# Optimization experiments

Hardware: AMD Instinct MI355X
Metric: run time of the kernel (lower is better)

Reference implementation:

```python
import jax, jax.numpy as jnp
from jax import lax
import numpy as np

B, T, IN_DIM = 32, 2048, 36
HIDDEN, CODE_DIM, N_CODES, STRIDE, N_RES = 256, 128, 1024, 4, 4
BETA = 0.25
GN_GROUPS = 8


def conv1d(x, w, b, stride=1, padding=0):
    # x: (B,C,T), w: (O,I,k) torch layout
    y = lax.conv_general_dilated(x, w, (stride,), [(padding, padding)],
                                 dimension_numbers=('NCH', 'OIH', 'NCH'))
    return y + b[None, :, None]


def conv_transpose1d(x, w, b, stride, padding):
    # torch ConvTranspose1d weight layout (in, out, k); output_padding=0 (stride even)
    k = w.shape[-1]
    w_t = jnp.transpose(jnp.flip(w, -1), (1, 0, 2))  # (out, in, k)
    y = lax.conv_general_dilated(x, w_t, (1,), [(k - 1 - padding, k - 1 - padding)],
                                 lhs_dilation=(stride,), dimension_numbers=('NCH', 'OIH', 'NCH'))
    return y + b[None, :, None]


def group_norm(x, gamma, beta, eps=1e-5):
    Bx, C, Tx = x.shape
    xg = x.reshape(Bx, GN_GROUPS, C // GN_GROUPS, Tx)
    mu = xg.mean(axis=(2, 3), keepdims=True)
    var = xg.var(axis=(2, 3), keepdims=True)
    xn = ((xg - mu) * lax.rsqrt(var + eps)).reshape(Bx, C, Tx)
    return xn * gamma[None, :, None] + beta[None, :, None]


def res_block(x, g1, be1, w1, b1, g2, be2, w2, b2):
    h = conv1d(jax.nn.silu(group_norm(x, g1, be1)), w1, b1, padding=1)
    h = conv1d(jax.nn.silu(group_norm(h, g2, be2)), w2, b2, padding=1)
    return x + h


def vq(z_e, codebook):
    # z_e: (B, C, K); nearest-neighbor + straight-through estimator
    Bx, C, K = z_e.shape
    z = z_e.transpose(0, 2, 1).reshape(-1, C)  # (B*K, C)
    dist = (z * z).sum(1, keepdims=True) + (codebook * codebook).sum(1)[None, :] - 2.0 * (z @ codebook.T)
    codes = jnp.argmin(dist, axis=1)  # (B*K,)
    z_q = codebook[codes].reshape(Bx, K, C).transpose(0, 2, 1)  # (B, C, K)
    z_q_st = z_e + lax.stop_gradient(z_q - z_e)
    loss_vq = jnp.mean((z_q - lax.stop_gradient(z_e)) ** 2) + BETA * jnp.mean((lax.stop_gradient(z_q) - z_e) ** 2)
    counts = jnp.zeros((N_CODES,), z_e.dtype).at[codes].add(1.0)
    avg = counts / z.shape[0]
    perplexity = jnp.exp(-jnp.sum(avg * jnp.log(avg + 1e-10)))
    return z_q_st, codes.reshape(Bx, K), loss_vq, perplexity


def _gather_pos(a):  # slices (0:18),(18:21),(27:30) -> 24 dims
    return jnp.concatenate([a[..., 0:18], a[..., 18:21], a[..., 27:30]], axis=-1)


def _gather_dir(a):  # slices (21:27),(30:36) -> 12 dims
    return jnp.concatenate([a[..., 21:27], a[..., 30:36]], axis=-1)


def setup_inputs() -> dict:
    ks = iter(jax.random.split(jax.random.key(0), 64))

    def nrm(shape, scale=1.0):
        return scale * jax.random.normal(next(ks), shape, jnp.float32)

    def cw(o, i, k):
        return nrm((o, i, k), 1.0 / np.sqrt(i * k))

    def rcw(n, o, i, k):
        return nrm((n, o, i, k), 1.0 / np.sqrt(i * k))

    inp = {
        'x': nrm((B, T, IN_DIM)),
        'hand_valid_mask': jax.random.uniform(next(ks), (B, T, 2), jnp.float32),
        'enc_in_w': cw(HIDDEN, IN_DIM, 3), 'enc_in_b': nrm((HIDDEN,), 0.01),
        'enc_gn1_g': 1.0 + nrm((N_RES, HIDDEN), 0.01), 'enc_gn1_b': nrm((N_RES, HIDDEN), 0.01),
        'enc_c1_w': rcw(N_RES, HIDDEN, HIDDEN, 3), 'enc_c1_b': nrm((N_RES, HIDDEN), 0.01),
        'enc_gn2_g': 1.0 + nrm((N_RES, HIDDEN), 0.01), 'enc_gn2_b': nrm((N_RES, HIDDEN), 0.01),
        'enc_c2_w': rcw(N_RES, HIDDEN, HIDDEN, 3), 'enc_c2_b': nrm((N_RES, HIDDEN), 0.01),
        'down_w': cw(HIDDEN, HIDDEN, 2 * STRIDE), 'down_b': nrm((HIDDEN,), 0.01),
        'enc_out_w': cw(CODE_DIM, HIDDEN, 1), 'enc_out_b': nrm((CODE_DIM,), 0.01),
        'codebook': jax.random.uniform(next(ks), (N_CODES, CODE_DIM), jnp.float32, -1.0 / N_CODES, 1.0 / N_CODES),
        'dec_in_w': cw(HIDDEN, CODE_DIM, 1), 'dec_in_b': nrm((HIDDEN,), 0.01),
        'up_w': nrm((HIDDEN, HIDDEN, 2 * STRIDE), 1.0 / np.sqrt(HIDDEN * 2 * STRIDE)), 'up_b': nrm((HIDDEN,), 0.01),
        'dec_gn1_g': 1.0 + nrm((N_RES, HIDDEN), 0.01), 'dec_gn1_b': nrm((N_RES, HIDDEN), 0.01),
        'dec_c1_w': rcw(N_RES, HIDDEN, HIDDEN, 3), 'dec_c1_b': nrm((N_RES, HIDDEN), 0.01),
        'dec_gn2_g': 1.0 + nrm((N_RES, HIDDEN), 0.01), 'dec_gn2_b': nrm((N_RES, HIDDEN), 0.01),
        'dec_c2_w': rcw(N_RES, HIDDEN, HIDDEN, 3), 'dec_c2_b': nrm((N_RES, HIDDEN), 0.01),
        'dec_out_w': cw(IN_DIM, HIDDEN, 3), 'dec_out_b': nrm((IN_DIM,), 0.01),
    }
    return inp


def reference(x, hand_valid_mask, enc_in_w, enc_in_b, enc_gn1_g, enc_gn1_b, enc_c1_w, enc_c1_b,
              enc_gn2_g, enc_gn2_b, enc_c2_w, enc_c2_b, down_w, down_b, enc_out_w, enc_out_b,
              codebook, dec_in_w, dec_in_b, up_w, up_b, dec_gn1_g, dec_gn1_b, dec_c1_w, dec_c1_b,
              dec_gn2_g, dec_gn2_b, dec_c2_w, dec_c2_b, dec_out_w, dec_out_b):
    Bx, Tx, _ = x.shape
    # ---- encode ----
    h = conv1d(x.transpose(0, 2, 1), enc_in_w, enc_in_b, padding=1)
    for i in range(N_RES):
        h = res_block(h, enc_gn1_g[i], enc_gn1_b[i], enc_c1_w[i], enc_c1_b[i],
                      enc_gn2_g[i], enc_gn2_b[i], enc_c2_w[i], enc_c2_b[i])
    h = conv1d(h, down_w, down_b, stride=STRIDE, padding=STRIDE // 2)
    z_e = conv1d(h, enc_out_w, enc_out_b)  # (B, CODE_DIM, K); latent mask is all-ones (no input_length)
    # ---- quantize ----
    z_q, codes, loss_vq, perplexity = vq(z_e, codebook)
    # ---- decode ----
    h = conv1d(z_q, dec_in_w, dec_in_b)
    h = conv_transpose1d(h, up_w, up_b, STRIDE, STRIDE // 2)
    for i in range(N_RES):
        h = res_block(h, dec_gn1_g[i], dec_gn1_b[i], dec_c1_w[i], dec_c1_b[i],
                      dec_gn2_g[i], dec_gn2_b[i], dec_c2_w[i], dec_c2_b[i])
    x_hat = conv1d(h, dec_out_w, dec_out_b, padding=1)[..., :Tx].transpose(0, 2, 1)  # (B,T,36)
    # ---- smooth-L1 position loss (mask of ones (B,T,1): denom = B*T) ----
    d = _gather_pos(x_hat) - _gather_pos(x)
    ad = jnp.abs(d)
    l1 = jnp.where(ad < 1.0, 0.5 * d * d, ad - 0.5)
    loss_recon_pos = l1.sum() / (Bx * Tx)
    # ---- cosine direction loss with hand validity mask ----
    x_vec = _gather_dir(x).reshape(Bx, Tx, 4, 3)
    h_vec = _gather_dir(x_hat).reshape(Bx, Tx, 4, 3)
    mL = hand_valid_mask[..., 0]
    mR = hand_valid_mask[..., 1]
    m_vec = jnp.stack([mL, mL, mR, mR], axis=-1)  # (B,T,4)
    eps = 1e-8
    xn = x_vec / (jnp.linalg.norm(x_vec, axis=-1, keepdims=True) + eps)
    hn = h_vec / (jnp.linalg.norm(h_vec, axis=-1, keepdims=True) + eps)
    cos = (xn * hn).sum(-1)
    loss_recon_dir = ((1.0 - cos) * m_vec).sum() / jnp.maximum(m_vec.sum(), 1.0)
    return x_hat, codes, loss_vq, perplexity, loss_recon_pos, loss_recon_dir
```

## Files before the change

kernel.cpp:

```cpp
#include <hip/hip_runtime.h>
#include <cstddef>
#include <cstdint>


#define TID ((int)threadIdx.x)
#define NB 32

__device__ __forceinline__ float silu_f(float y) { return y / (1.f + expf(-y)); }

__global__ void perm_oik_iko(const float* __restrict__ src, float* __restrict__ dst,
                             int R, int O, int I, int K) {
  int n = R * O * I * K;
  for (int idx = blockIdx.x * blockDim.x + TID; idx < n; idx += gridDim.x * blockDim.x) {
    int o = idx % O;
    int k = (idx / O) % K;
    int i = (idx / (O * K)) % I;
    int r = idx / (O * K * I);
    dst[idx] = src[((r * O + o) * I + i) * K + k];
  }
}

__global__ void perm_decout(const float* __restrict__ src, float* __restrict__ dst) {
  int n = 256 * 36 * 4;
  for (int idx = blockIdx.x * blockDim.x + TID; idx < n; idx += gridDim.x * blockDim.x) {
    int k = idx & 3;
    int o = (idx >> 2) % 36;
    int i = idx / 144;
    dst[idx] = (k < 3) ? src[(o * 256 + i) * 3 + k] : 0.f;
  }
}

__global__ void zero_k(float* p, int n) {
  int i = blockIdx.x * blockDim.x + TID;
  if (i < n) p[i] = 0.f;
}

__global__ void csq_f32(const float* __restrict__ cb, float* __restrict__ csq) {
  int j = blockIdx.x * blockDim.x + TID;
  if (j < 1024) {
    float s = 0.f;
    for (int c = 0; c < 128; c++) { float v = cb[j * 128 + c]; s += v * v; }
    csq[j] = s;
  }
}

__global__ __launch_bounds__(256) void conv_in_k(const float* __restrict__ x, const float* __restrict__ wT,
                                                 const float* __restrict__ bias, float* __restrict__ out,
                                                 float* __restrict__ partOut) {
  int b = blockIdx.x >> 5;
  int t0 = (blockIdx.x & 31) << 6;
  int o0 = blockIdx.y << 6;
  int tx = TID & 15, oy = TID >> 4;
  __shared__ float ins[36][68];
  __shared__ float wsl[36 * 192];
  for (int idx = TID; idx < 36 * 66; idx += 256) {
    int i = idx % 36, c = idx / 36;
    int t = t0 - 1 + c;
    float v = 0.f;
    if (t >= 0 && t < 2048) v = x[((size_t)(b * 2048 + t)) * 36 + i];
    ins[i][c] = v;
  }
  for (int idx = TID; idx < 36 * 192; idx += 256) {
    int o = idx & 63;
    int kk = (idx >> 6) % 3;
    int i = idx / 192;
    wsl[idx] = wT[(i * 3 + kk) * 256 + o0 + o];
  }
  __syncthreads();
  float acc[4][4];
#pragma unroll
  for (int m = 0; m < 4; m++)
#pragma unroll
    for (int n = 0; n < 4; n++) acc[m][n] = 0.f;
  for (int i = 0; i < 36; i++) {
    float xv[6];
    float4 x4 = *(const float4*)&ins[i][tx << 2];
    xv[0] = x4.x; xv[1] = x4.y; xv[2] = x4.z; xv[3] = x4.w;
    xv[4] = ins[i][(tx << 2) + 4];
    xv[5] = ins[i][(tx << 2) + 5];
    const float* wrow = &wsl[i * 192];
    float wv[3][4];
    *(float4*)wv[0] = *(const float4*)&wrow[oy << 2];
    *(float4*)wv[1] = *(const float4*)&wrow[64 + (oy << 2)];
    *(float4*)wv[2] = *(const float4*)&wrow[128 + (oy << 2)];
#pragma unroll
    for (int m = 0; m < 4; m++)
#pragma unroll
      for (int n = 0; n < 4; n++)
        acc[m][n] = fmaf(wv[0][m], xv[n], fmaf(wv[1][m], xv[n + 1], fmaf(wv[2][m], xv[n + 2], acc[m][n])));
  }
  int obase = o0 + (oy << 2);
  float s1 = 0.f, s2 = 0.f;
#pragma unroll
  for (int m = 0; m < 4; m++) {
    int o = obase + m;
    float bv = bias[o];
    size_t rowo = (((size_t)((b << 8) + o)) << 11) + t0 + (tx << 2);
#pragma unroll
    for (int n = 0; n < 4; n++) {
      float v = acc[m][n] + bv;
      out[rowo + n] = v;
      s1 += v; s2 += v * v;
    }
  }
  __syncthreads();
  float* red = (float*)ins;
  red[TID] = s1; red[256 + TID] = s2;
  __syncthreads();
  for (int st = 64; st > 0; st >>= 1) {
    if ((TID & 127) < st) { red[TID] += red[TID + st]; red[256 + TID] += red[256 + TID + st]; }
    __syncthreads();
  }
  if ((TID & 127) == 0) {
    int g = (blockIdx.y << 1) + (TID >> 7);
    atomicAdd(&partOut[(((b << 3) + g) << 1)], red[TID]);
    atomicAdd(&partOut[(((b << 3) + g) << 1) + 1], red[256 + TID]);
  }
}

__global__ __launch_bounds__(256, 2) void conv3_gn_k(const float* __restrict__ in, const float* __restrict__ partIn,
                                                     const float* __restrict__ gamma, const float* __restrict__ beta,
                                                     const float* __restrict__ wT, const float* __restrict__ bias,
                                                     const float* __restrict__ src, float* __restrict__ out,
                                                     float* __restrict__ partOut) {
  int b = blockIdx.x >> 3;
  int t0 = (blockIdx.x & 7) << 8;
  int o0 = blockIdx.y << 7;
  int tx = TID & 15, oy = TID >> 4;
  __shared__ float ins[16][264];
  __shared__ float wsl[3 * 16 * 128];
  float acc[2][4][16];
#pragma unroll
  for (int h = 0; h < 2; h++)
#pragma unroll
    for (int m = 0; m < 4; m++)
#pragma unroll
      for (int n = 0; n < 16; n++) acc[h][m][n] = 0.f;
  for (int ic0 = 0; ic0 < 256; ic0 += 16) {
    int g = ic0 >> 5;
    const float* pp = partIn + (((size_t)((b << 3) + g)) << 1);
    float s1 = pp[0], s2 = pp[1];
    float mu = s1 * (1.f / 65536.f);
    float var = s2 * (1.f / 65536.f) - mu * mu;
    float rs = rsqrtf(var + 1e-5f);
    __syncthreads();
    {
      int ch = ic0 + oy;
      float a = rs * gamma[ch];
      float bb = beta[ch] - mu * a;
      const float* grow = in + (((size_t)((b << 8) + ch)) << 11);
#pragma unroll
      for (int q = 0; q < 17; q++) {
        int c = tx + (q << 4);
        if (c < 260) {
          int t = t0 - 1 + c;
          float v = 0.f;
          if (t >= 0 && t < 2048) {
            float h = grow[t];
            float y = h * a + bb;
            v = y / (1.f + expf(-y));
          }
          ins[oy][c] = v;
        }
      }
    }
    for (int idx4 = TID; idx4 < 1536; idx4 += 256) {
      int o4 = (idx4 & 31) << 2;
      int i = (idx4 >> 5) & 15;
      int kk = idx4 >> 9;
      *(float4*)&wsl[(((kk << 4) + i) << 7) + o4] =
          *(const float4*)&wT[((ic0 + i) * 3 + kk) * 256 + o0 + o4];
    }
    __syncthreads();
    for (int i = 0; i < 16; i++) {
      float xq[4][6];
#pragma unroll
      for (int q = 0; q < 4; q++) {
        *(float4*)&xq[q][0] = *(const float4*)&ins[i][(q << 6) + (tx << 2)];
        *(float2*)&xq[q][4] = *(const float2*)&ins[i][(q << 6) + (tx << 2) + 4];
      }
      float wv[3][4], wb[3][4];
#pragma unroll
      for (int kk = 0; kk < 3; kk++) {
        const float* wrow = &wsl[((kk << 4) + i) << 7];
        *(float4*)wv[kk] = *(const float4*)&wrow[oy << 2];
        *(float4*)wb[kk] = *(const float4*)&wrow[64 + (oy << 2)];
      }
#pragma unroll
      for (int m = 0; m < 4; m++)
#pragma unroll
        for (int q = 0; q < 4; q++)
#pragma unroll
          for (int n = 0; n < 4; n++) {
            acc[0][m][(q << 2) + n] =
                fmaf(wv[0][m], xq[q][n], fmaf(wv[1][m], xq[q][n + 1], fmaf(wv[2][m], xq[q][n + 2], acc[0][m][(q << 2) + n])));
            acc[1][m][(q << 2) + n] =
                fmaf(wb[0][m], xq[q][n], fmaf(wb[1][m], xq[q][n + 1], fmaf(wb[2][m], xq[q][n + 2], acc[1][m][(q << 2) + n])));
          }
    }
  }
  float sh1[2] = {0.f, 0.f}, sh2[2] = {0.f, 0.f};
#pragma unroll
  for (int h = 0; h < 2; h++)
#pragma unroll
    for (int m = 0; m < 4; m++) {
      int o = o0 + (h << 6) + (oy << 2) + m;
      float bv = bias[o];
      size_t rowbase = (((size_t)((b << 8) + o)) << 11) + t0 + (tx << 2);
#pragma unroll
      for (int q = 0; q < 4; q++) {
        size_t row = rowbase + (q << 6);
#pragma unroll
        for (int n = 0; n < 4; n++) {
          float v = acc[h][m][(q << 2) + n] + bv;
          if (src) v += src[row + n];
          out[row + n] = v;
          sh1[h] += v; sh2[h] += v * v;
        }
      }
    }
  if (partOut) {
    __syncthreads();
    float* red = (float*)ins;
#pragma unroll
    for (int h = 0; h < 2; h++) {
      red[TID] = sh1[h]; red[256 + TID] = sh2[h];
      __syncthreads();
      for (int st = 64; st > 0; st >>= 1) {
        if ((TID & 127) < st) { red[TID] += red[TID + st]; red[256 + TID] += red[256 + TID + st]; }
        __syncthreads();
      }
      if ((TID & 127) == 0) {
        int g = (blockIdx.y << 2) + (h << 1) + (TID >> 7);
        atomicAdd(&partOut[(((b << 3) + g) << 1)], red[TID]);
        atomicAdd(&partOut[(((b << 3) + g) << 1) + 1], red[256 + TID]);
      }
      __syncthreads();
    }
  }
}

__global__ __launch_bounds__(256) void conv_down_k(const float* __restrict__ in, const float* __restrict__ wT,
                                                   const float* __restrict__ bias, float* __restrict__ out) {
  int b = blockIdx.x >> 3;
  int to0 = (blockIdx.x & 7) << 6;
  int o0 = blockIdx.y << 6;
  int tx = TID & 15, oy = TID >> 4;
  __shared__ float ins[16][264];
  __shared__ float wsl[16 * 512];
  float acc[4][4];
#pragma unroll
  for (int m = 0; m < 4; m++)
#pragma unroll
    for (int n = 0; n < 4; n++) acc[m][n] = 0.f;
  for (int ic0 = 0; ic0 < 256; ic0 += 16) {
    __syncthreads();
    for (int idx = TID; idx < 16 * 260; idx += 256) {
      int r = idx / 260, c = idx % 260;
      int s = (to0 << 2) - 2 + c;
      float v = 0.f;
      if (s >= 0 && s < 2048) v = in[(((size_t)((b << 8) + ic0 + r)) << 11) + s];
      ins[r][c] = v;
    }
    for (int idx = TID; idx < 16 * 512; idx += 256) {
      int o = idx & 63;
      int kk = (idx >> 6) & 7;
      int i = idx >> 9;
      wsl[idx] = wT[((ic0 + i) * 8 + kk) * 256 + o0 + o];
    }
    __syncthreads();
#pragma unroll 2
    for (int i = 0; i < 16; i++) {
      float xv[20];
#pragma unroll
      for (int q = 0; q < 5; q++) *(float4*)&xv[q * 4] = *(const float4*)&ins[i][(tx << 4) + (q << 2)];
      float wv[8][4];
#pragma unroll
      for (int kk = 0; kk < 8; kk++) *(float4*)wv[kk] = *(const float4*)&wsl[(i << 9) + (kk << 6) + (oy << 2)];
#pragma unroll
      for (int n = 0; n < 4; n++)
#pragma unroll
        for (int kk = 0; kk < 8; kk++) {
          float xval = xv[(n << 2) + kk];
#pragma unroll
          for (int m = 0; m < 4; m++) acc[m][n] = fmaf(wv[kk][m], xval, acc[m][n]);
        }
    }
  }
  int obase = o0 + (oy << 2);
#pragma unroll
  for (int m = 0; m < 4; m++) {
    int o = obase + m;
    float bv = bias[o];
    size_t rowo = (((size_t)((b << 8) + o)) << 9) + to0 + (tx << 2);
#pragma unroll
    for (int n = 0; n < 4; n++) out[rowo + n] = acc[m][n] + bv;
  }
}

__global__ __launch_bounds__(256) void conv1x1_k(const float* __restrict__ in, const float* __restrict__ wIO,
                                                 const float* __restrict__ bias, float* __restrict__ out,
                                                 int Kc, int O) {
  int b = blockIdx.x >> 3;
  int t0 = (blockIdx.x & 7) << 6;
  int o0 = blockIdx.y << 6;
  int tx = TID & 15, oy = TID >> 4;
  __shared__ float xs[32][64];
  __shared__ float wsd[32][64];
  float acc[4][4];
#pragma unroll
  for (int m = 0; m < 4; m++)
#pragma unroll
    for (int n = 0; n < 4; n++) acc[m][n] = 0.f;
  for (int ic0 = 0; ic0 < Kc; ic0 += 32) {
    __syncthreads();
    for (int idx = TID; idx < 2048; idx += 256) {
      int r = idx >> 6, c = idx & 63;
      xs[r][c] = in[((size_t)(b * Kc + ic0 + r) << 9) + t0 + c];
      wsd[r][c] = wIO[(ic0 + r) * O + o0 + c];
    }
    __syncthreads();
#pragma unroll 8
    for (int i = 0; i < 32; i++) {
      float4 xvv = *(const float4*)&xs[i][tx << 2];
      float4 wvv = *(const float4*)&wsd[i][oy << 2];
      float xv[4] = {xvv.x, xvv.y, xvv.z, xvv.w};
      float wv[4] = {wvv.x, wvv.y, wvv.z, wvv.w};
#pragma unroll
      for (int m = 0; m < 4; m++)
#pragma unroll
        for (int n = 0; n < 4; n++) acc[m][n] = fmaf(wv[m], xv[n], acc[m][n]);
    }
  }
#pragma unroll
  for (int m = 0; m < 4; m++) {
    int o = o0 + (oy << 2) + m;
    float bv = bias[o];
    size_t rowo = ((size_t)(b * O + o) << 9) + t0 + (tx << 2);
#pragma unroll
    for (int n = 0; n < 4; n++) out[rowo + n] = acc[m][n] + bv;
  }
}

__global__ __launch_bounds__(256) void vq_tiled(const float* __restrict__ zE,
                                                const float* __restrict__ cb,
                                                const float* __restrict__ csq,
                                                int* __restrict__ codes) {
  int b = blockIdx.x >> 3;
  int t0 = (blockIdx.x & 7) << 6;
  int cq = TID & 15, pq = TID >> 4;
  __shared__ float Zs[128][66];
  __shared__ float Cs[64][129];
  __shared__ float zsqs[64];
  __shared__ float bd[64][17];
  __shared__ int bix[64][17];
  for (int idx = TID; idx < 128 * 64; idx += 256) {
    int c = idx >> 6, p = idx & 63;
    Zs[c][p] = zE[((size_t)(b * 128 + c) << 9) + t0 + p];
  }
  __syncthreads();
  if (TID < 64) {
    float s = 0.f;
    for (int c = 0; c < 128; c++) { float v = Zs[c][TID]; s += v * v; }
    zsqs[TID] = s;
  }
  float best[4];
  int bidx[4];
#pragma unroll
  for (int n = 0; n < 4; n++) { best[n] = 3.4e38f; bidx[n] = 0; }
  const int j0 = cq << 2;
  for (int cg = 0; cg < 16; cg++) {
    __syncthreads();
    for (int idx = TID; idx < 64 * 128; idx += 256) {
      int j = idx >> 7, c = idx & 127;
      Cs[j][c] = cb[((cg << 6) + j) * 128 + c];
    }
    __syncthreads();
    float acc[4][4];
#pragma unroll
    for (int u = 0; u < 4; u++)
#pragma unroll
      for (int n = 0; n < 4; n++) acc[u][n] = 0.f;
    for (int c = 0; c < 128; c++) {
      float4 zv4 = *(const float4*)&Zs[c][pq << 2];
      float zv[4] = {zv4.x, zv4.y, zv4.z, zv4.w};
      float cv[4];
#pragma unroll
      for (int u = 0; u < 4; u++) cv[u] = Cs[j0 + u][c];
#pragma unroll
      for (int u = 0; u < 4; u++)
#pragma unroll
        for (int n = 0; n < 4; n++) acc[u][n] += zv[n] * cv[u];
    }
#pragma unroll
    for (int u = 0; u < 4; u++) {
      int code = (cg << 6) + j0 + u;
      float cs_ = csq[code];
#pragma unroll
      for (int n = 0; n < 4; n++) {
        float A = zsqs[(pq << 2) + n] + cs_;
        float B = 2.0f * acc[u][n];
        float d = A - B;
        if (d < best[n]) { best[n] = d; bidx[n] = code; }
      }
    }
  }
  __syncthreads();
#pragma unroll
  for (int n = 0; n < 4; n++) { bd[(pq << 2) + n][cq] = best[n]; bix[(pq << 2) + n][cq] = bidx[n]; }
  __syncthreads();
  if (TID < 64) {
    float bb = bd[TID][0];
    int bj = bix[TID][0];
    for (int q = 1; q < 16; q++) {
      float d = bd[TID][q];
      int j = bix[TID][q];
      if (d < bb || (d == bb && j < bj)) { bb = d; bj = j; }
    }
    codes[(b << 9) + t0 + TID] = bj;
  }
}

__global__ void count_k(const int* __restrict__ codes, float* __restrict__ counts) {
  int n = blockIdx.x * blockDim.x + TID;
  if (n < 16384) atomicAdd(&counts[codes[n]], 1.f);
}

__global__ __launch_bounds__(256) void gather_k(const float* __restrict__ cb, const int* __restrict__ codes,
                                                const float* __restrict__ zE, float* __restrict__ zQ,
                                                float* __restrict__ vqsum) {
  double part = 0.;
  const int total = 32 * 128 * 512;
  for (int idx = blockIdx.x * blockDim.x + TID; idx < total; idx += gridDim.x * blockDim.x) {
    int t = idx & 511;
    int c = (idx >> 9) & 127;
    int b = idx >> 16;
    int code = codes[(b << 9) + t];
    float q = cb[code * 128 + c];
    double d = (double)q - (double)zE[idx];
    zQ[idx] = q;
    part += d * d;
  }
  __shared__ double red[256];
  red[TID] = part;
  __syncthreads();
  for (int st = 128; st > 0; st >>= 1) {
    if (TID < st) red[TID] += red[TID + st];
    __syncthreads();
  }
  if (TID == 0) atomicAdd(vqsum, (float)red[0]);
}

__global__ __launch_bounds__(256) void conv_up_k(const float* __restrict__ in, const float* __restrict__ w,
                                                 const float* __restrict__ bias, float* __restrict__ out,
                                                 float* __restrict__ partOut) {
  int b = blockIdx.x / 17;
  int s0 = (blockIdx.x % 17) << 5;
  int o0 = blockIdx.y << 6;
  int tx = TID & 15, oy = TID >> 4;
  __shared__ float ins[16][36];
  __shared__ float wsl[16 * 512];
  float acc[2][4][4];
#pragma unroll
  for (int j = 0; j < 2; j++)
#pragma unroll
    for (int m = 0; m < 4; m++)
#pragma unroll
      for (int r = 0; r < 4; r++) acc[j][m][r] = 0.f;
  for (int ic0 = 0; ic0 < 256; ic0 += 16) {
    __syncthreads();
    for (int idx = TID; idx < 16 * 34; idx += 256) {
      int r = idx / 34, c = idx % 34;
      int s = s0 - 1 + c;
      float v = 0.f;
      if (s >= 0 && s < 512) v = in[(((size_t)((b << 8) + ic0 + r)) << 9) + s];
      ins[r][c] = v;
    }
    for (int idx = TID; idx < 8192; idx += 256) {
      int rr = idx & 3;
      int o = (idx >> 2) & 63;
      int h = (idx >> 8) & 1;
      int i = idx >> 9;
      wsl[idx] = w[(((size_t)(ic0 + i)) << 11) + ((size_t)(o0 + o) << 3) + (h << 2) + rr];
    }
    __syncthreads();
#pragma unroll 2
    for (int i = 0; i < 16; i++) {
      float x0 = ins[i][2 * tx], x1 = ins[i][2 * tx + 1], x2 = ins[i][2 * tx + 2];
#pragma unroll
      for (int m = 0; m < 4; m++) {
        int om = (oy << 2) + m;
        float4 wa4 = *(const float4*)&wsl[(i << 9) + (om << 2)];
        float4 wb4 = *(const float4*)&wsl[(i << 9) + 256 + (om << 2)];
        float wa[4] = {wa4.x, wa4.y, wa4.z, wa4.w};
        float wb[4] = {wb4.x, wb4.y, wb4.z, wb4.w};
#pragma unroll
        for (int r = 0; r < 4; r++) {
          acc[0][m][r] = fmaf(x1, wa[r], fmaf(x0, wb[r], acc[0][m][r]));
          acc[1][m][r] = fmaf(x2, wa[r], fmaf(x1, wb[r], acc[1][m][r]));
        }
      }
    }
  }
  float s1 = 0.f, s2 = 0.f;
#pragma unroll
  for (int j = 0; j < 2; j++) {
    int sS = s0 + (tx << 1) + j;
#pragma unroll
    for (int m = 0; m < 4; m++) {
      int o = o0 + (oy << 2) + m;
      float bv = bias[o];
#pragma unroll
      for (int r = 0; r < 4; r++) {
        int t = (sS << 2) + r - 2;
        if (t >= 0 && t < 2048) {
          float v = acc[j][m][r] + bv;
          out[(((size_t)((b << 8) + o)) << 11) + t] = v;
          s1 += v; s2 += v * v;
        }
      }
    }
  }
  __syncthreads();
  float* red = (float*)ins;
  red[TID] = s1; red[256 + TID] = s2;
  __syncthreads();
  for (int st = 64; st > 0; st >>= 1) {
    if ((TID & 127) < st) { red[TID] += red[TID + st]; red[256 + TID] += red[256 + TID + st]; }
    __syncthreads();
  }
  if ((TID & 127) == 0) {
    int g = (blockIdx.y << 1) + (TID >> 7);
    atomicAdd(&partOut[(((b << 3) + g) << 1)], red[TID]);
    atomicAdd(&partOut[(((b << 3) + g) << 1) + 1], red[256 + TID]);
  }
}

__global__ __launch_bounds__(256) void conv_out_k(const float* __restrict__ in, const float* __restrict__ wP,
                                                  const float* __restrict__ bias, float* __restrict__ xhat) {
  int b = blockIdx.x >> 5;
  int t0 = (blockIdx.x & 31) << 6;
  int tx = TID & 63, oy = TID >> 6;
  __shared__ float ins[32][68];
  __shared__ float wsl[32 * 144];
  float acc[9];
#pragma unroll
  for (int m = 0; m < 9; m++) acc[m] = 0.f;
  for (int ic0 = 0; ic0 < 256; ic0 += 32) {
    __syncthreads();
    for (int idx = TID; idx < 32 * 66; idx += 256) {
      int r = idx / 66, c = idx % 66;
      int t = t0 - 1 + c;
      float v = 0.f;
      if (t >= 0 && t < 2048) v = in[(((size_t)((b << 8) + ic0 + r)) << 11) + t];
      ins[r][c] = v;
    }
    for (int idx = TID; idx < 32 * 144; idx += 256) {
      wsl[idx] = wP[ic0 * 144 + idx];
    }
    __syncthreads();
#pragma unroll 4
    for (int i = 0; i < 32; i++) {
      float x0 = ins[i][tx], x1 = ins[i][tx + 1], x2 = ins[i][tx + 2];
#pragma unroll
      for (int m = 0; m < 9; m++) {
        int o = oy * 9 + m;
        float4 wv = *(const float4*)&wsl[(i * 36 + o) << 2];
        acc[m] = fmaf(wv.x, x0, fmaf(wv.y, x1, fmaf(wv.z, x2, acc[m])));
      }
    }
  }
  size_t orow = ((size_t)(b << 11) + t0 + tx) * 36;
#pragma unroll
  for (int m = 0; m < 9; m++) {
    int o = oy * 9 + m;
    xhat[orow + o] = acc[m] + bias[o];
  }
}

__global__ __launch_bounds__(256) void loss_k(const float* __restrict__ x, const float* __restrict__ xh,
                                              const float* __restrict__ mask, float* __restrict__ scal) {
  float pos = 0.f, dir = 0.f, ms = 0.f;
  for (int n = blockIdx.x * blockDim.x + TID; n < 65536; n += gridDim.x * blockDim.x) {
    const float* xp = x + (size_t)n * 36;
    const float* hp = xh + (size_t)n * 36;
    float a[36], h[36];
#pragma unroll
    for (int d4 = 0; d4 < 36; d4 += 4) {
      *(float4*)&a[d4] = *(const float4*)&xp[d4];
      *(float4*)&h[d4] = *(const float4*)&hp[d4];
    }
#pragma unroll
    for (int d = 0; d < 36; d++) {
      if (d < 21 || (d >= 27 && d < 30)) {
        float df = h[d] - a[d];
        float ad = fabsf(df);
        pos += (ad < 1.f) ? 0.5f * df * df : ad - 0.5f;
      }
    }
    float mL = mask[2 * (size_t)n], mR = mask[2 * (size_t)n + 1];
    const int vb[4] = {21, 24, 30, 33};
    float mv[4] = {mL, mL, mR, mR};
#pragma unroll
    for (int v = 0; v < 4; v++) {
      int o = vb[v];
      float ax = a[o], ay = a[o + 1], az = a[o + 2];
      float hx = h[o], hy = h[o + 1], hz = h[o + 2];
      float an = sqrtf(ax * ax + ay * ay + az * az) + 1e-8f;
      float hn = sqrtf(hx * hx + hy * hy + hz * hz) + 1e-8f;
      float cs = (ax * hx + ay * hy + az * hz) / (an * hn);
      dir += (1.f - cs) * mv[v];
    }
    ms += 2.f * (mL + mR);
  }
  __shared__ float rp[256], rd[256], rm[256];
  rp[TID] = pos; rd[TID] = dir; rm[TID] = ms;
  __syncthreads();
  for (int st = 128; st > 0; st >>= 1) {
    if (TID < st) { rp[TID] += rp[TID + st]; rd[TID] += rd[TID + st]; rm[TID] += rm[TID + st]; }
    __syncthreads();
  }
  if (TID == 0) {
    atomicAdd(&scal[1], rp[0]);
    atomicAdd(&scal[2], rd[0]);
    atomicAdd(&scal[3], rm[0]);
  }
}

__global__ __launch_bounds__(256) void finalize_k(const float* __restrict__ counts, const float* __restrict__ scal,
                                                  float* __restrict__ tail) {
  __shared__ float red[256];
  float s = 0.f;
  for (int j = TID; j < 1024; j += 256) {
    float avg = counts[j] * (1.f / 16384.f);
    s += avg * logf(avg + 1e-10f);
  }
  red[TID] = s;
  __syncthreads();
  for (int st = 128; st > 0; st >>= 1) {
    if (TID < st) red[TID] += red[TID + st];
    __syncthreads();
  }
  if (TID == 0) {
    tail[0] = 1.25f * scal[0] * (1.f / 2097152.f);
    tail[1] = expf(-red[0]);
    tail[2] = scal[1] * (1.f / 65536.f);
    tail[3] = scal[2] / fmaxf(scal[3], 1.f);
  }
}

__global__ void codesf_k(const int* __restrict__ codes, float* __restrict__ o) {
  int n = blockIdx.x * blockDim.x + TID;
  if (n < 16384) o[n] = (float)codes[n];
}

extern "C" void kernel_launch(void* const* d_in, const int* in_sizes, int n_in,
                              void* d_out, int out_size, void* d_ws, size_t ws_size,
                              hipStream_t stream) {
  const float* x = (const float*)d_in[0];
  const float* mask = (const float*)d_in[1];
  const float* enc_in_w = (const float*)d_in[2];
  const float* enc_in_b = (const float*)d_in[3];
  const float* enc_gn1_g = (const float*)d_in[4];
  const float* enc_gn1_b = (const float*)d_in[5];
  const float* enc_c1_w = (const float*)d_in[6];
  const float* enc_c1_b = (const float*)d_in[7];
  const float* enc_gn2_g = (const float*)d_in[8];
  const float* enc_gn2_b = (const float*)d_in[9];
  const float* enc_c2_w = (const float*)d_in[10];
  const float* enc_c2_b = (const float*)d_in[11];
  const float* down_w = (const float*)d_in[12];
  const float* down_b = (const float*)d_in[13];
  const float* enc_out_w = (const float*)d_in[14];
  const float* enc_out_b = (const float*)d_in[15];
  const float* codebook = (const float*)d_in[16];
  const float* dec_in_w = (const float*)d_in[17];
  const float* dec_in_b = (const float*)d_in[18];
  const float* up_w = (const float*)d_in[19];
  const float* up_b = (const float*)d_in[20];
  const float* dec_gn1_g = (const float*)d_in[21];
  const float* dec_gn1_b = (const float*)d_in[22];
  const float* dec_c1_w = (const float*)d_in[23];
  const float* dec_c1_b = (const float*)d_in[24];
  const float* dec_gn2_g = (const float*)d_in[25];
  const float* dec_gn2_b = (const float*)d_in[26];
  const float* dec_c2_w = (const float*)d_in[27];
  const float* dec_c2_b = (const float*)d_in[28];
  const float* dec_out_w = (const float*)d_in[29];
  const float* dec_out_b = (const float*)d_in[30];

  char* W = (char*)d_ws;
  float* zE = (float*)(W + 0);
  float* zQ = (float*)(W + 8388608);
  int* codes = (int*)(W + 16777216);
  float* counts = (float*)(W + 16842752);
  float* scal = (float*)(W + 16846848);
  float* stats = (float*)(W + 16846880);
  float* csq = (float*)(W + 16883744);
  float* wf_enc_in = (float*)(W + 16887840);
  float* wf_enc_c1 = (float*)(W + 16998432);
  float* wf_enc_c2 = (float*)(W + 20144160);
  float* wf_down = (float*)(W + 23289888);
  float* wf_enc_out = (float*)(W + 25387040);
  float* wf_dec_in = (float*)(W + 25518112);
  float* wf_dec_c1 = (float*)(W + 25649184);
  float* wf_dec_c2 = (float*)(W + 28794912);
  float* wf_dec_out = (float*)(W + 31940640);
  float* f0 = (float*)(W + 50331648);
  float* f2 = (float*)(W + 50331648 + (size_t)67108864);
  float* dech = (float*)(W + 50331648 + 2 * (size_t)67108864);

  dim3 blk(256);
  zero_k<<<dim3(41), blk, 0, stream>>>(counts, 1024 + 8 + 9216);
  perm_oik_iko<<<dim3(128), blk, 0, stream>>>(enc_in_w, wf_enc_in, 1, 256, 36, 3);
  perm_oik_iko<<<dim3(1024), blk, 0, stream>>>(enc_c1_w, wf_enc_c1, 4, 256, 256, 3);
  perm_oik_iko<<<dim3(1024), blk, 0, stream>>>(enc_c2_w, wf_enc_c2, 4, 256, 256, 3);
  perm_oik_iko<<<dim3(1024), blk, 0, stream>>>(down_w, wf_down, 1, 256, 256, 8);
  perm_oik_iko<<<dim3(128), blk, 0, stream>>>(enc_out_w, wf_enc_out, 1, 128, 256, 1);
  perm_oik_iko<<<dim3(128), blk, 0, stream>>>(dec_in_w, wf_dec_in, 1, 256, 128, 1);
  perm_oik_iko<<<dim3(1024), blk, 0, stream>>>(dec_c1_w, wf_dec_c1, 4, 256, 256, 3);
  perm_oik_iko<<<dim3(1024), blk, 0, stream>>>(dec_c2_w, wf_dec_c2, 4, 256, 256, 3);
  perm_decout<<<dim3(64), blk, 0, stream>>>(dec_out_w, wf_dec_out);
  csq_f32<<<dim3(4), blk, 0, stream>>>(codebook, csq);

  conv_in_k<<<dim3(NB * 32, 4), blk, 0, stream>>>(x, wf_enc_in, enc_in_b, f0, stats + 0 * 512);
  for (int i = 0; i < 4; i++) {
    float* sIn = stats + (2 * i) * 512;
    float* sMid = stats + (2 * i + 1) * 512;
    float* sOut = (i < 3) ? stats + (2 * i + 2) * 512 : nullptr;
    conv3_gn_k<<<dim3(NB * 8, 2), blk, 0, stream>>>(f0, sIn, enc_gn1_g + i * 256, enc_gn1_b + i * 256,
                                                    wf_enc_c1 + i * 196608, enc_c1_b + i * 256, nullptr, f2, sMid);
    conv3_gn_k<<<dim3(NB * 8, 2), blk, 0, stream>>>(f2, sMid, enc_gn2_g + i * 256, enc_gn2_b + i * 256,
                                                    wf_enc_c2 + i * 196608, enc_c2_b + i * 256, f0, f0, sOut);
  }
  conv_down_k<<<dim3(NB * 8, 4), blk, 0, stream>>>(f0, wf_down, down_b, f2);
  conv1x1_k<<<dim3(NB * 8, 2), blk, 0, stream>>>(f2, wf_enc_out, enc_out_b, zE, 256, 128);

  vq_tiled<<<dim3(256), blk, 0, stream>>>(zE, codebook, csq, codes);
  count_k<<<dim3(64), blk, 0, stream>>>(codes, counts);
  gather_k<<<dim3(512), blk, 0, stream>>>(codebook, codes, zE, zQ, &scal[0]);

  float* xhat = (float*)d_out;
  conv1x1_k<<<dim3(NB * 8, 4), blk, 0, stream>>>(zQ, wf_dec_in, dec_in_b, dech, 128, 256);
  conv_up_k<<<dim3(NB * 17, 4), blk, 0, stream>>>(dech, up_w, up_b, f0, stats + 9 * 512);
  for (int i = 0; i < 4; i++) {
    float* sIn = stats + (9 + 2 * i) * 512;
    float* sMid = stats + (10 + 2 * i) * 512;
    float* sOut = (i < 3) ? stats + (11 + 2 * i) * 512 : nullptr;
    conv3_gn_k<<<dim3(NB * 8, 2), blk, 0, stream>>>(f0, sIn, dec_gn1_g + i * 256, dec_gn1_b + i * 256,
                                                    wf_dec_c1 + i * 196608, dec_c1_b + i * 256, nullptr, f2, sMid);
    conv3_gn_k<<<dim3(NB * 8, 2), blk, 0, stream>>>(f2, sMid, dec_gn2_g + i * 256, dec_gn2_b + i * 256,
                                                    wf_dec_c2 + i * 196608, dec_c2_b + i * 256, f0, f0, sOut);
  }
  conv_out_k<<<dim3(NB * 32), blk, 0, stream>>>(f0, wf_dec_out, dec_out_b, xhat);

  loss_k<<<dim3(256), blk, 0, stream>>>(x, xhat, mask, scal);
  finalize_k<<<dim3(1), blk, 0, stream>>>(counts, scal, (float*)d_out + 2375680);
  codesf_k<<<dim3(64), blk, 0, stream>>>(codes, (float*)d_out + 2359296);
}
```

Measured before the change: 6.664 ms.

## Pad conv3 weight smem, restripe down/up conv tiles, fuse VQ count and code cast

Pads the conv3 shared weight rows to 140 floats with a skew, so the two float4 weight reads per thread fall in different LDS banks. Changes conv_down's time mapping to interleave threads at stride 4 so shared reads and global stores are contiguous across lanes. Widens conv_up tiles to 64 input steps per block (fewer blocks, more outputs per thread). Folds the code histogram atomics and the int-to-float code cast into the VQ kernel, removing two launches, at the cost of more atomic contention inside vq_tiled.

New measurement: 6.653 ms. About the same (-0.2%).

```diff
diff --git a/kernel.cpp b/kernel.cpp
--- a/kernel.cpp
+++ b/kernel.cpp
@@ -118,6 +118,7 @@
   }
 }
 
+#define WROW 140
 __global__ __launch_bounds__(256, 2) void conv3_gn_k(const float* __restrict__ in, const float* __restrict__ partIn,
                                                      const float* __restrict__ gamma, const float* __restrict__ beta,
                                                      const float* __restrict__ wT, const float* __restrict__ bias,
@@ -128,7 +129,7 @@
   int o0 = blockIdx.y << 7;
   int tx = TID & 15, oy = TID >> 4;
   __shared__ float ins[16][264];
-  __shared__ float wsl[3 * 16 * 128];
+  __shared__ float wsl[3 * 16 * WROW];
   float acc[2][4][16];
 #pragma unroll
   for (int h = 0; h < 2; h++)
@@ -136,6 +137,7 @@
     for (int m = 0; m < 4; m++)
 #pragma unroll
       for (int n = 0; n < 16; n++) acc[h][m][n] = 0.f;
+  const int ro = (oy << 2) + ((oy >> 3) << 2);
   for (int ic0 = 0; ic0 < 256; ic0 += 16) {
     int g = ic0 >> 5;
     const float* pp = partIn + (((size_t)((b << 3) + g)) << 1);
@@ -168,7 +170,8 @@
       int o4 = (idx4 & 31) << 2;
       int i = (idx4 >> 5) & 15;
       int kk = idx4 >> 9;
-      *(float4*)&wsl[(((kk << 4) + i) << 7) + o4] =
+      int po = o4 + ((o4 >> 5) << 2);
+      *(float4*)&wsl[((kk << 4) + i) * WROW + po] =
           *(const float4*)&wT[((ic0 + i) * 3 + kk) * 256 + o0 + o4];
     }
     __syncthreads();
@@ -182,9 +185,9 @@
       float wv[3][4], wb[3][4];
 #pragma unroll
       for (int kk = 0; kk < 3; kk++) {
-        const float* wrow = &wsl[((kk << 4) + i) << 7];
-        *(float4*)wv[kk] = *(const float4*)&wrow[oy << 2];
-        *(float4*)wb[kk] = *(const float4*)&wrow[64 + (oy << 2)];
+        const float* wrow = &wsl[((kk << 4) + i) * WROW];
+        *(float4*)wv[kk] = *(const float4*)&wrow[ro];
+        *(float4*)wb[kk] = *(const float4*)&wrow[72 + ro];
       }
 #pragma unroll
       for (int m = 0; m < 4; m++)
@@ -252,7 +255,7 @@
 #pragma unroll
   for (int m = 0; m < 4; m++)
 #pragma unroll
-    for (int n = 0; n < 4; n++) acc[m][n] = 0.f;
+    for (int u = 0; u < 4; u++) acc[m][u] = 0.f;
   for (int ic0 = 0; ic0 < 256; ic0 += 16) {
     __syncthreads();
     for (int idx = TID; idx < 16 * 260; idx += 256) {
@@ -271,19 +274,22 @@
     __syncthreads();
 #pragma unroll 2
     for (int i = 0; i < 16; i++) {
-      float xv[20];
-#pragma unroll
-      for (int q = 0; q < 5; q++) *(float4*)&xv[q * 4] = *(const float4*)&ins[i][(tx << 4) + (q << 2)];
+      float xv[4][8];
+#pragma unroll
+      for (int u = 0; u < 4; u++) {
+        *(float4*)&xv[u][0] = *(const float4*)&ins[i][(u << 6) + (tx << 2)];
+        *(float4*)&xv[u][4] = *(const float4*)&ins[i][(u << 6) + (tx << 2) + 4];
+      }
       float wv[8][4];
 #pragma unroll
       for (int kk = 0; kk < 8; kk++) *(float4*)wv[kk] = *(const float4*)&wsl[(i << 9) + (kk << 6) + (oy << 2)];
 #pragma unroll
-      for (int n = 0; n < 4; n++)
+      for (int u = 0; u < 4; u++)
 #pragma unroll
         for (int kk = 0; kk < 8; kk++) {
-          float xval = xv[(n << 2) + kk];
-#pragma unroll
-          for (int m = 0; m < 4; m++) acc[m][n] = fmaf(wv[kk][m], xval, acc[m][n]);
+          float xval = xv[u][kk];
+#pragma unroll
+          for (int m = 0; m < 4; m++) acc[m][u] = fmaf(wv[kk][m], xval, acc[m][u]);
         }
     }
   }
@@ -292,9 +298,9 @@
   for (int m = 0; m < 4; m++) {
     int o = obase + m;
     float bv = bias[o];
-    size_t rowo = (((size_t)((b << 8) + o)) << 9) + to0 + (tx << 2);
-#pragma unroll
-    for (int n = 0; n < 4; n++) out[rowo + n] = acc[m][n] + bv;
+    size_t rowo = (((size_t)((b << 8) + o)) << 9) + to0 + tx;
+#pragma unroll
+    for (int u = 0; u < 4; u++) out[rowo + (u << 4)] = acc[m][u] + bv;
   }
 }
 
@@ -345,7 +351,9 @@
 __global__ __launch_bounds__(256) void vq_tiled(const float* __restrict__ zE,
                                                 const float* __restrict__ cb,
                                                 const float* __restrict__ csq,
-                                                int* __restrict__ codes) {
+                                                int* __restrict__ codes,
+                                                float* __restrict__ counts,
+                                                float* __restrict__ codesF) {
   int b = blockIdx.x >> 3;
   int t0 = (blockIdx.x & 7) << 6;
   int cq = TID & 15, pq = TID >> 4;
@@ -417,13 +425,11 @@
       int j = bix[TID][q];
       if (d < bb || (d == bb && j < bj)) { bb = d; bj = j; }
     }
-    codes[(b << 9) + t0 + TID] = bj;
-  }
-}
-
-__global__ void count_k(const int* __restrict__ codes, float* __restrict__ counts) {
-  int n = blockIdx.x * blockDim.x + TID;
-  if (n < 16384) atomicAdd(&counts[codes[n]], 1.f);
+    int n = (b << 9) + t0 + TID;
+    codes[n] = bj;
+    codesF[n] = (float)bj;
+    atomicAdd(&counts[bj], 1.f);
+  }
 }
 
 __global__ __launch_bounds__(256) void gather_k(const float* __restrict__ cb, const int* __restrict__ codes,
@@ -454,23 +460,23 @@
 __global__ __launch_bounds__(256) void conv_up_k(const float* __restrict__ in, const float* __restrict__ w,
                                                  const float* __restrict__ bias, float* __restrict__ out,
                                                  float* __restrict__ partOut) {
-  int b = blockIdx.x / 17;
-  int s0 = (blockIdx.x % 17) << 5;
+  int b = blockIdx.x / 9;
+  int s0 = (blockIdx.x % 9) << 6;
   int o0 = blockIdx.y << 6;
   int tx = TID & 15, oy = TID >> 4;
-  __shared__ float ins[16][36];
+  __shared__ float ins[16][68];
   __shared__ float wsl[16 * 512];
-  float acc[2][4][4];
-#pragma unroll
-  for (int j = 0; j < 2; j++)
+  float acc[4][4][4];
+#pragma unroll
+  for (int j = 0; j < 4; j++)
 #pragma unroll
     for (int m = 0; m < 4; m++)
 #pragma unroll
       for (int r = 0; r < 4; r++) acc[j][m][r] = 0.f;
   for (int ic0 = 0; ic0 < 256; ic0 += 16) {
     __syncthreads();
-    for (int idx = TID; idx < 16 * 34; idx += 256) {
-      int r = idx / 34, c = idx % 34;
+    for (int idx = TID; idx < 16 * 66; idx += 256) {
+      int r = idx / 66, c = idx % 66;
       int s = s0 - 1 + c;
       float v = 0.f;
       if (s >= 0 && s < 512) v = in[(((size_t)((b << 8) + ic0 + r)) << 9) + s];
@@ -486,7 +492,9 @@
     __syncthreads();
 #pragma unroll 2
     for (int i = 0; i < 16; i++) {
-      float x0 = ins[i][2 * tx], x1 = ins[i][2 * tx + 1], x2 = ins[i][2 * tx + 2];
+      float xv[5];
+#pragma unroll
+      for (int q = 0; q < 5; q++) xv[q] = ins[i][(tx << 2) + q];
 #pragma unroll
       for (int m = 0; m < 4; m++) {
         int om = (oy << 2) + m;
@@ -495,17 +503,17 @@
         float wa[4] = {wa4.x, wa4.y, wa4.z, wa4.w};
         float wb[4] = {wb4.x, wb4.y, wb4.z, wb4.w};
 #pragma unroll
-        for (int r = 0; r < 4; r++) {
-          acc[0][m][r] = fmaf(x1, wa[r], fmaf(x0, wb[r], acc[0][m][r]));
-          acc[1][m][r] = fmaf(x2, wa[r], fmaf(x1, wb[r], acc[1][m][r]));
-        }
+        for (int j = 0; j < 4; j++)
+#pragma unroll
+          for (int r = 0; r < 4; r++)
+            acc[j][m][r] = fmaf(xv[j + 1], wa[r], fmaf(xv[j], wb[r], acc[j][m][r]));
       }
     }
   }
   float s1 = 0.f, s2 = 0.f;
 #pragma unroll
-  for (int j = 0; j < 2; j++) {
-    int sS = s0 + (tx << 1) + j;
+  for (int j = 0; j < 4; j++) {
+    int sS = s0 + (tx << 2) + j;
 #pragma unroll
     for (int m = 0; m < 4; m++) {
       int o = o0 + (oy << 2) + m;
@@ -647,11 +655,6 @@
     tail[2] = scal[1] * (1.f / 65536.f);
     tail[3] = scal[2] / fmaxf(scal[3], 1.f);
   }
-}
-
-__global__ void codesf_k(const int* __restrict__ codes, float* __restrict__ o) {
-  int n = blockIdx.x * blockDim.x + TID;
-  if (n < 16384) o[n] = (float)codes[n];
 }
 
 extern "C" void kernel_launch(void* const* d_in, const int* in_sizes, int n_in,
@@ -736,13 +739,12 @@
   conv_down_k<<<dim3(NB * 8, 4), blk, 0, stream>>>(f0, wf_down, down_b, f2);
   conv1x1_k<<<dim3(NB * 8, 2), blk, 0, stream>>>(f2, wf_enc_out, enc_out_b, zE, 256, 128);
 
-  vq_tiled<<<dim3(256), blk, 0, stream>>>(zE, codebook, csq, codes);
-  count_k<<<dim3(64), blk, 0, stream>>>(codes, counts);
+  vq_tiled<<<dim3(256), blk, 0, stream>>>(zE, codebook, csq, codes, counts, (float*)d_out + 2359296);
   gather_k<<<dim3(512), blk, 0, stream>>>(codebook, codes, zE, zQ, &scal[0]);
 
   float* xhat = (float*)d_out;
   conv1x1_k<<<dim3(NB * 8, 4), blk, 0, stream>>>(zQ, wf_dec_in, dec_in_b, dech, 128, 256);
-  conv_up_k<<<dim3(NB * 17, 4), blk, 0, stream>>>(dech, up_w, up_b, f0, stats + 9 * 512);
+  conv_up_k<<<dim3(NB * 9, 4), blk, 0, stream>>>(dech, up_w, up_b, f0, stats + 9 * 512);
   for (int i = 0; i < 4; i++) {
     float* sIn = stats + (9 + 2 * i) * 512;
     float* sMid = stats + (10 + 2 * i) * 512;
@@ -756,5 +758,4 @@
 
   loss_k<<<dim3(256), blk, 0, stream>>>(x, xhat, mask, scal);
   finalize_k<<<dim3(1), blk, 0, stream>>>(counts, scal, (float*)d_out + 2375680);
-  codesf_k<<<dim3(64), blk, 0, stream>>>(codes, (float*)d_out + 2359296);
-}
+}
```
